# Performance work log

Measured on AMD Instinct MI355X. Metric: run time of the kernel, lower is better.

Reference implementation:

```python
import jax, jax.numpy as jnp
import numpy as np

ALPHA = 0.5  # ent message step size
BETA = 0.5   # rel message step size
N_ENT, N_REL, D, E = 100000, 500, 128, 1000000
EPS = 1e-12  # tf.math.l2_normalize epsilon


def _mul_complex(x, y):
    # interleaved complex multiply: even idx = real, odd idx = imag (RotatE)
    xr, xi = x[:, ::2], x[:, 1::2]
    yr, yi = y[:, ::2], y[:, 1::2]
    rr = xr * yr - xi * yi
    ri = xi * yr + xr * yi
    return jnp.stack([rr, ri], axis=2).reshape(x.shape[0], -1)


def _l2_normalize_pairs(r):
    # tf.math.l2_normalize over each (real, imag) pair
    r2 = r.reshape(-1, 2)
    denom = jnp.sqrt(jnp.maximum(jnp.sum(r2 * r2, axis=1, keepdims=True), EPS))
    return (r2 / denom).reshape(r.shape)


def setup_inputs() -> dict:
    key = jax.random.key(0)
    k = jax.random.split(key, 7)
    return {
        "ent_emb": jax.random.normal(k[0], (N_ENT, D), dtype=jnp.float32),
        "rel_emb": jax.random.normal(k[1], (N_REL, D), dtype=jnp.float32),
        "ent_invsum": jax.random.uniform(k[2], (N_ENT, 1), dtype=jnp.float32),
        "rel_invsum": jax.random.uniform(k[3], (N_REL, 1), dtype=jnp.float32),
        "head": jax.random.randint(k[4], (E,), 0, N_ENT, dtype=jnp.int32),
        "rel_idx": jax.random.randint(k[5], (E,), 0, N_REL, dtype=jnp.int32),
        "tail": jax.random.randint(k[6], (E,), 0, N_ENT, dtype=jnp.int32),
    }


def reference(ent_emb, rel_emb, ent_invsum, rel_invsum, head, rel_idx, tail):
    # RotatE mode: normalize each complex component of relation embeddings
    rel_n = _l2_normalize_pairs(rel_emb)

    def loss_fn(e, r):
        h = e[head]            # [E, D] gather
        t = e[tail]            # [E, D] gather
        rg = r[rel_idx]        # [E, D] gather
        return -jnp.sum((_mul_complex(h, rg) - t) ** 2)

    # tf.gradients(loss, [ent_emb, rel_emb]) -> scatter-add messages
    ent_msg, rel_msg = jax.grad(loss_fn, argnums=(0, 1))(ent_emb, rel_n)

    out_ent = jax.nn.relu(ent_emb + ALPHA * ent_invsum * ent_msg)
    out_rel = jax.nn.relu(rel_n + BETA * rel_invsum * rel_msg)
    return out_ent, out_rel
```

## Files before the change

kernel.cpp:

```cpp
#include <hip/hip_runtime.h>

#define N_ENT   100000
#define N_REL   500
#define DIM     128
#define NPAIR   64
#define CAP_E   36
#define NREP    8
#define CAP_RR  344
#define BIN_SH  5
#define NBIN    (N_ENT >> BIN_SH)
#define CAP_B   152
#define BS_THR  1024
#define MAXE    8
#define NCOPY   8
#define ALPHA   0.5f
#define BETA    0.5f
#define EPS_N   1e-12f
#define PMASK   0x1FFFFu
#define PAYMASK 0x03FFFFFFu
#define INVALID 0xFFFFFFFFu

__device__ __forceinline__ unsigned get_xcc() {
    unsigned x;
    asm("s_getreg_b32 %0, hwreg(HW_REG_XCC_ID)" : "=s"(x));
    return x & (NREP - 1u);
}

__device__ __forceinline__ unsigned pack_bf16(float2 v) {
    unsigned rx = __float_as_uint(v.x);
    unsigned ry = __float_as_uint(v.y);
    rx = (rx + 0x7FFFu + ((rx >> 16) & 1u)) >> 16;
    ry = (ry + 0x7FFFu + ((ry >> 16) & 1u)) & 0xFFFF0000u;
    return rx | ry;
}
__device__ __forceinline__ float2 unpack_bf16(unsigned u) {
    float2 v;
    v.x = __uint_as_float(u << 16);
    v.y = __uint_as_float(u & 0xFFFF0000u);
    return v;
}

__device__ __forceinline__ unsigned short pack_fp8(float2 v) {
    int p = __builtin_amdgcn_cvt_pk_fp8_f32(v.x, v.y, 0, false);
    return (unsigned short)(p & 0xFFFF);
}
__device__ __forceinline__ float2 unpack_fp8(unsigned short u) {
    float2 v;
    v.x = __builtin_amdgcn_cvt_f32_fp8((int)u, 0);
    v.y = __builtin_amdgcn_cvt_f32_fp8((int)u, 1);
    return v;
}

__global__ void zero_kernel(float* p, int n) {
    int i = blockIdx.x * blockDim.x + threadIdx.x;
    if (i < n) p[i] = 0.0f;
}

__global__ void cvt_ent_kernel(const float* __restrict__ ent, unsigned short* __restrict__ ent_f8, int npairs) {
    int i = blockIdx.x * blockDim.x + threadIdx.x;
    if (i >= npairs) return;
    ent_f8[i] = pack_fp8(reinterpret_cast<const float2*>(ent)[i]);
}

__global__ void rel_norm_kernel(const float* __restrict__ rel, float* __restrict__ rel_n,
                                unsigned* __restrict__ rel_bf, int npairs) {
    int i = blockIdx.x * blockDim.x + threadIdx.x;
    if (i >= npairs) return;
    float2 v = reinterpret_cast<const float2*>(rel)[i];
    float d = sqrtf(fmaxf(v.x * v.x + v.y * v.y, EPS_N));
    float2 o; o.x = v.x / d; o.y = v.y / d;
    reinterpret_cast<float2*>(rel_n)[i] = o;
    rel_bf[i] = pack_bf16(o);
}


__global__ __launch_bounds__(BS_THR) void bin_scatter(
                            const int* __restrict__ head,
                            const int* __restrict__ relidx,
                            const int* __restrict__ tail,
                            unsigned* __restrict__ bin_cnt,
                            unsigned* __restrict__ bins,
                            unsigned* __restrict__ deg_r,
                            uint2*    __restrict__ list_r,
                            int n_edge) {
    __shared__ unsigned lcnt[NBIN];
    __shared__ unsigned lbase[NBIN];
    __shared__ unsigned rcnt[N_REL];
    __shared__ unsigned rbase[N_REL];
    int tid = threadIdx.x;

    for (int i = tid; i < NBIN; i += BS_THR) lcnt[i] = 0;
    for (int i = tid; i < N_REL; i += BS_THR) rcnt[i] = 0;
    __syncthreads();

    int e0 = blockIdx.x * (MAXE * BS_THR);

    unsigned eh[MAXE], er[MAXE], et[MAXE];
#pragma unroll
    for (int i = 0; i < MAXE; ++i) {
        int e = e0 + tid + i * BS_THR;
        if (e < n_edge) {
            eh[i] = (unsigned)head[e];
            er[i] = (unsigned)relidx[e];
            et[i] = (unsigned)tail[e];
        } else {
            eh[i] = INVALID; er[i] = 0; et[i] = 0;
        }
    }

#pragma unroll
    for (int i = 0; i < MAXE; ++i) {
        if (eh[i] != INVALID) {
            atomicAdd(&lcnt[et[i] >> BIN_SH], 1u);
            atomicAdd(&lcnt[eh[i] >> BIN_SH], 1u);
            atomicAdd(&rcnt[er[i]], 1u);
        }
    }
    __syncthreads();

    unsigned rep = get_xcc();
    for (int b = tid; b < NBIN; b += BS_THR) {
        unsigned c = lcnt[b];
        if (c) lbase[b] = __hip_atomic_fetch_add(&bin_cnt[rep * NBIN + b], c,
                                                 __ATOMIC_RELAXED, __HIP_MEMORY_SCOPE_WORKGROUP);
    }
    for (int b = tid; b < N_REL; b += BS_THR) {
        unsigned c = rcnt[b];
        if (c) rbase[b] = __hip_atomic_fetch_add(&deg_r[rep * N_REL + b], c,
                                                 __ATOMIC_RELAXED, __HIP_MEMORY_SCOPE_WORKGROUP);
    }
    __syncthreads();

#pragma unroll
    for (int i = 0; i < MAXE; ++i) {
        if (eh[i] == INVALID) continue;
        unsigned h = eh[i], r = er[i], t = et[i];

        unsigned bt = t >> BIN_SH;
        unsigned s1 = lbase[bt] + (atomicSub(&lcnt[bt], 1u) - 1u);
        if (s1 < CAP_B) bins[((size_t)rep * NBIN + bt) * CAP_B + s1] = ((t & 31u) << 27) | (r << 17) | h;

        unsigned bh = h >> BIN_SH;
        unsigned s2 = lbase[bh] + (atomicSub(&lcnt[bh], 1u) - 1u);
        if (s2 < CAP_B) bins[((size_t)rep * NBIN + bh) * CAP_B + s2] = ((h & 31u) << 27) | (1u << 26) | (r << 17) | t;

        unsigned s3 = rbase[r] + (atomicSub(&rcnt[r], 1u) - 1u);
        if (s3 < CAP_RR) list_r[((size_t)rep * N_REL + r) * CAP_RR + s3] = make_uint2(h, t);
    }
}

__global__ void fused_ent(const float* __restrict__ ent,
                          const unsigned short* __restrict__ ent_f8,
                          const unsigned* __restrict__ rel_bf,
                          const unsigned* __restrict__ bin_cnt,
                          const unsigned* __restrict__ bins,
                          const float* __restrict__ ent_inv,
                          float* __restrict__ out_ent) {
    __shared__ unsigned cnt[32][2];
    __shared__ unsigned slots[32][2][CAP_E];
    int bin = blockIdx.x;
    int tid = threadIdx.x;

    if (tid < 64) cnt[tid >> 1][tid & 1] = 0;
    __syncthreads();

    for (int rep = 0; rep < NREP; ++rep) {
        int bn = (int)min(bin_cnt[(size_t)rep * NBIN + bin], (unsigned)CAP_B);
        for (int k = tid; k < bn; k += blockDim.x) {
            unsigned entry = bins[((size_t)rep * NBIN + bin) * CAP_B + k];
            unsigned el   = entry >> 27;
            unsigned role = (entry >> 26) & 1u;
            unsigned pay  = entry & PAYMASK;
            unsigned p = atomicAdd(&cnt[el][role], 1u);
            if (p < CAP_E) slots[el][role][p] = pay;
        }
    }
    __syncthreads();

    int wid  = tid >> 6;
    int lane = tid & 63;
    const float2* ent2 = reinterpret_cast<const float2*>(ent);

    for (int s = 0; s < 8; ++s) {
        int el = wid * 8 + s;
        int e  = (bin << BIN_SH) + el;
        int dt = (int)min(cnt[el][0], (unsigned)CAP_E);
        int dh = (int)min(cnt[el][1], (unsigned)CAP_E);

        float2 acc = make_float2(0.f, 0.f);
        for (int j = 0; j < dt; ++j) {
            unsigned ep = slots[el][0][j];
            float2 hv = unpack_fp8(ent_f8[(size_t)(ep & PMASK) * NPAIR + lane]);
            float2 rv = unpack_bf16(rel_bf[(size_t)(ep >> 17) * NPAIR + lane]);
            acc.x += hv.x * rv.x - hv.y * rv.y;
            acc.y += hv.y * rv.x + hv.x * rv.y;
        }
        for (int j = 0; j < dh; ++j) {
            unsigned ep = slots[el][1][j];
            float2 tv = unpack_fp8(ent_f8[(size_t)(ep & PMASK) * NPAIR + lane]);
            float2 rv = unpack_bf16(rel_bf[(size_t)(ep >> 17) * NPAIR + lane]);
            acc.x += tv.x * rv.x + tv.y * rv.y;
            acc.y += tv.y * rv.x - tv.x * rv.y;
        }

        float2 ev = ent2[(size_t)e * NPAIR + lane];
        float degf = (float)(dt + dh);
        float a = ALPHA * ent_inv[e];
        float2 o;
        o.x = fmaxf(ev.x + a * 2.f * (acc.x - degf * ev.x), 0.f);
        o.y = fmaxf(ev.y + a * 2.f * (acc.y - degf * ev.y), 0.f);
        reinterpret_cast<float2*>(out_ent)[(size_t)e * NPAIR + lane] = o;
    }
}

__global__ void rel_pass8(const unsigned short* __restrict__ ent_f8,
                          const unsigned* __restrict__ deg_r,
                          const uint2* __restrict__ list_r,
                          float* __restrict__ rel_part) {
    __shared__ float sh[4][NPAIR][3];
    int r   = blockIdx.x >> 3;
    int rep = blockIdx.x & 7;
    int wid = threadIdx.x >> 6;
    int lane = threadIdx.x & 63;
    int nr = (int)min(deg_r[(size_t)rep * N_REL + r], (unsigned)CAP_RR);

    const uint2* seg = list_r + ((size_t)rep * N_REL + r) * CAP_RR;

    float2 T0 = make_float2(0.f, 0.f), T1 = make_float2(0.f, 0.f);
    float S0 = 0.f, S1 = 0.f;
    for (int k = wid * 2; k < nr; k += 8) {
        uint2 e0 = seg[k];
        float2 hv0 = unpack_fp8(ent_f8[(size_t)e0.x * NPAIR + lane]);
        float2 tv0 = unpack_fp8(ent_f8[(size_t)e0.y * NPAIR + lane]);
        if (k + 1 < nr) {
            uint2 e1 = seg[k + 1];
            float2 hv1 = unpack_fp8(ent_f8[(size_t)e1.x * NPAIR + lane]);
            float2 tv1 = unpack_fp8(ent_f8[(size_t)e1.y * NPAIR + lane]);
            S1   += hv1.x * hv1.x + hv1.y * hv1.y;
            T1.x += tv1.x * hv1.x + tv1.y * hv1.y;
            T1.y += tv1.y * hv1.x - tv1.x * hv1.y;
        }
        S0   += hv0.x * hv0.x + hv0.y * hv0.y;
        T0.x += tv0.x * hv0.x + tv0.y * hv0.y;
        T0.y += tv0.y * hv0.x - tv0.x * hv0.y;
    }
    sh[wid][lane][0] = T0.x + T1.x;
    sh[wid][lane][1] = T0.y + T1.y;
    sh[wid][lane][2] = S0 + S1;
    __syncthreads();
    if (wid == 0) {
        float tx = 0.f, ty = 0.f, s = 0.f;
#pragma unroll
        for (int w = 0; w < 4; ++w) {
            tx += sh[w][lane][0];
            ty += sh[w][lane][1];
            s  += sh[w][lane][2];
        }
        size_t o = (((size_t)r * NREP + rep) * NPAIR + lane) * 3;
        rel_part[o + 0] = tx;
        rel_part[o + 1] = ty;
        rel_part[o + 2] = s;
    }
}

__global__ void rel_fin(const float* __restrict__ rel_n,
                        const float* __restrict__ rel_part,
                        const float* __restrict__ rel_inv,
                        float* __restrict__ out_rel) {
    int r = blockIdx.x;
    int lane = threadIdx.x;
    float tx = 0.f, ty = 0.f, s = 0.f;
#pragma unroll
    for (int rep = 0; rep < NREP; ++rep) {
        size_t o = (((size_t)r * NREP + rep) * NPAIR + lane) * 3;
        tx += rel_part[o + 0];
        ty += rel_part[o + 1];
        s  += rel_part[o + 2];
    }
    float2 rn = reinterpret_cast<const float2*>(rel_n)[(size_t)r * NPAIR + lane];
    float b = BETA * rel_inv[r];
    float2 o2;
    o2.x = fmaxf(rn.x + b * (-2.f) * (rn.x * s - tx), 0.f);
    o2.y = fmaxf(rn.y + b * (-2.f) * (rn.y * s - ty), 0.f);
    reinterpret_cast<float2*>(out_rel)[(size_t)r * NPAIR + lane] = o2;
}


__global__ void rel_norm_only(const float* __restrict__ rel, float* __restrict__ rel_n, int npairs) {
    int i = blockIdx.x * blockDim.x + threadIdx.x;
    if (i >= npairs) return;
    float2 v = reinterpret_cast<const float2*>(rel)[i];
    float d = sqrtf(fmaxf(v.x * v.x + v.y * v.y, EPS_N));
    float2 o; o.x = v.x / d; o.y = v.y / d;
    reinterpret_cast<float2*>(rel_n)[i] = o;
}

__global__ void edge_kernel(const float* __restrict__ ent,
                            const float* __restrict__ rel_n,
                            const int* __restrict__ head,
                            const int* __restrict__ relidx,
                            const int* __restrict__ tail,
                            float* __restrict__ ent_msg,
                            float* __restrict__ rel_msg,
                            int n_edge) {
    int gid  = blockIdx.x * blockDim.x + threadIdx.x;
    int eid  = gid >> 6;
    int lane = threadIdx.x & 63;
    if (eid >= n_edge) return;

    int h = head[eid];
    int t = tail[eid];
    int r = relidx[eid];

    float2 hv = reinterpret_cast<const float2*>(ent)[(size_t)h * 64 + lane];
    float2 tv = reinterpret_cast<const float2*>(ent)[(size_t)t * 64 + lane];
    float2 rv = reinterpret_cast<const float2*>(rel_n)[(size_t)r * 64 + lane];

    float mr = hv.x * rv.x - hv.y * rv.y;
    float mi = hv.y * rv.x + hv.x * rv.y;
    float dr = mr - tv.x;
    float di = mi - tv.y;

    atomicAdd(&ent_msg[(size_t)t * DIM + 2 * lane],     2.0f * dr);
    atomicAdd(&ent_msg[(size_t)t * DIM + 2 * lane + 1], 2.0f * di);
    atomicAdd(&ent_msg[(size_t)h * DIM + 2 * lane],     -2.0f * (dr * rv.x + di * rv.y));
    atomicAdd(&ent_msg[(size_t)h * DIM + 2 * lane + 1], -2.0f * (di * rv.x - dr * rv.y));

    float* rm = rel_msg + (size_t)(blockIdx.x & (NCOPY - 1)) * (N_REL * DIM);
    atomicAdd(&rm[(size_t)r * DIM + 2 * lane],     -2.0f * (dr * hv.x + di * hv.y));
    atomicAdd(&rm[(size_t)r * DIM + 2 * lane + 1], -2.0f * (di * hv.x - dr * hv.y));
}

__global__ void fin_ent_kernel(const float* __restrict__ ent,
                               const float* __restrict__ invsum,
                               float* __restrict__ out, int nvec4) {
    int i = blockIdx.x * blockDim.x + threadIdx.x;
    if (i >= nvec4) return;
    int row = i >> 5;
    float a = ALPHA * invsum[row];
    float4 m = reinterpret_cast<const float4*>(out)[i];
    float4 e = reinterpret_cast<const float4*>(ent)[i];
    float4 o;
    o.x = fmaxf(e.x + a * m.x, 0.0f);
    o.y = fmaxf(e.y + a * m.y, 0.0f);
    o.z = fmaxf(e.z + a * m.z, 0.0f);
    o.w = fmaxf(e.w + a * m.w, 0.0f);
    reinterpret_cast<float4*>(out)[i] = o;
}

__global__ void fin_rel_kernel(const float* __restrict__ rel_n,
                               const float* __restrict__ invsum,
                               const float* __restrict__ rel_msg,
                               float* __restrict__ out, int n) {
    int i = blockIdx.x * blockDim.x + threadIdx.x;
    if (i >= n) return;
    int row = i >> 7;
    float s = 0.0f;
#pragma unroll
    for (int c = 0; c < NCOPY; ++c) s += rel_msg[(size_t)c * (N_REL * DIM) + i];
    float o = rel_n[i] + BETA * invsum[row] * s;
    out[i] = fmaxf(o, 0.0f);
}

extern "C" void kernel_launch(void* const* d_in, const int* in_sizes, int n_in,
                              void* d_out, int out_size, void* d_ws, size_t ws_size,
                              hipStream_t stream) {
    const float* ent     = (const float*)d_in[0];
    const float* rel     = (const float*)d_in[1];
    const float* ent_inv = (const float*)d_in[2];
    const float* rel_inv = (const float*)d_in[3];
    const int*   head    = (const int*)d_in[4];
    const int*   relidx  = (const int*)d_in[5];
    const int*   tail    = (const int*)d_in[6];

    const int n_edge = in_sizes[4];

    float* out     = (float*)d_out;
    float* out_ent = out;
    float* out_rel = out + (size_t)N_ENT * DIM;

    const int B = 256;

    const size_t W_RELN  = 0;
    const size_t W_RELB  = W_RELN + (size_t)N_REL * NPAIR * 2;
    const size_t W_ENTF8 = W_RELB + (size_t)N_REL * NPAIR;
    const size_t W_BCNT  = W_ENTF8 + (size_t)N_ENT * NPAIR / 2;
    const size_t W_DEGR  = W_BCNT + (size_t)NREP * NBIN;
    const size_t W_RPART = W_DEGR + (size_t)NREP * N_REL;
    const size_t W_BINS  = W_RPART + (size_t)N_REL * NREP * NPAIR * 3;
    const size_t W_LISTR = W_BINS + (size_t)NREP * NBIN * CAP_B;
    const size_t W_END   = W_LISTR + (size_t)NREP * N_REL * CAP_RR * 2;
    const size_t need_fast = W_END * 4;

    float* ws = (float*)d_ws;

    if (ws_size >= need_fast) {
        float*          rel_n    = ws + W_RELN;
        unsigned*       rel_bf   = (unsigned*)(ws + W_RELB);
        unsigned short* ent_f8   = (unsigned short*)(ws + W_ENTF8);
        unsigned*       bin_cnt  = (unsigned*)(ws + W_BCNT);
        unsigned*       deg_r    = (unsigned*)(ws + W_DEGR);
        float*          rel_part = ws + W_RPART;
        unsigned*       bins     = (unsigned*)(ws + W_BINS);
        uint2*          list_r   = (uint2*)(ws + W_LISTR);

        hipMemsetAsync((void*)bin_cnt, 0,
                       (size_t)(NREP * NBIN + NREP * N_REL) * 4, stream);

        {
            int np = N_ENT * NPAIR;
            cvt_ent_kernel<<<(np + B - 1) / B, B, 0, stream>>>(ent, ent_f8, np);
        }
        {
            int npairs = N_REL * NPAIR;
            rel_norm_kernel<<<(npairs + B - 1) / B, B, 0, stream>>>(rel, rel_n, rel_bf, npairs);
        }
        {
            int nblk = (n_edge + MAXE * BS_THR - 1) / (MAXE * BS_THR);
            bin_scatter<<<nblk, BS_THR, 0, stream>>>(
                head, relidx, tail, bin_cnt, bins, deg_r, list_r, n_edge);
        }

        fused_ent<<<NBIN, B, 0, stream>>>(ent, ent_f8, rel_bf, bin_cnt, bins,
                                          ent_inv, out_ent);
        rel_pass8<<<N_REL * NREP, B, 0, stream>>>(ent_f8, deg_r, list_r, rel_part);
        rel_fin<<<N_REL, 64, 0, stream>>>(rel_n, rel_part, rel_inv, out_rel);
    } else {
        float* rel_n   = ws;
        float* rel_msg = ws + N_REL * DIM;

        {
            int n = N_ENT * DIM;
            zero_kernel<<<(n + B - 1) / B, B, 0, stream>>>(out_ent, n);
            int m = NCOPY * N_REL * DIM;
            zero_kernel<<<(m + B - 1) / B, B, 0, stream>>>(rel_msg, m);
        }
        {
            int npairs = N_REL * NPAIR;
            rel_norm_only<<<(npairs + B - 1) / B, B, 0, stream>>>(rel, rel_n, npairs);
        }
        {
            long long threads = (long long)n_edge * 64;
            int blocks = (int)((threads + B - 1) / B);
            edge_kernel<<<blocks, B, 0, stream>>>(ent, rel_n, head, relidx, tail,
                                                  out_ent, rel_msg, n_edge);
        }
        {
            int nvec4 = N_ENT * (DIM / 4);
            fin_ent_kernel<<<(nvec4 + B - 1) / B, B, 0, stream>>>(ent, ent_inv, out_ent, nvec4);
            int n = N_REL * DIM;
            fin_rel_kernel<<<(n + B - 1) / B, B, 0, stream>>>(rel_n, rel_inv, rel_msg, out_rel, n);
        }
    }
}
```

Baseline: 220.0 us.

## Widen per-lane loads in fused_ent and fp8 conversion; split edges across half-waves

fused_ent now has each half-wavefront handle alternate edges, with each lane loading two complex pairs (ushort2 fp8, uint2 bf16). The two halves are combined with a cross-half shuffle before a float4 write of the output row. The goal is fewer, wider memory transactions and two independent edge gathers in flight per wave. The fp8 conversion kernel now packs four floats per thread into one dword, and MAXE drops from 8 to 4, which doubles the number of bin_scatter blocks. The costs are an extra shuffle reduction, half the lanes sitting idle during the epilogue, and load imbalance when edge counts are odd.

```diff
diff --git a/kernel.cpp b/kernel.cpp
--- a/kernel.cpp
+++ b/kernel.cpp
@@ -11,7 +11,7 @@
 #define NBIN    (N_ENT >> BIN_SH)
 #define CAP_B   152
 #define BS_THR  1024
-#define MAXE    8
+#define MAXE    4
 #define NCOPY   8
 #define ALPHA   0.5f
 #define BETA    0.5f
@@ -40,10 +40,6 @@
     return v;
 }
 
-__device__ __forceinline__ unsigned short pack_fp8(float2 v) {
-    int p = __builtin_amdgcn_cvt_pk_fp8_f32(v.x, v.y, 0, false);
-    return (unsigned short)(p & 0xFFFF);
-}
 __device__ __forceinline__ float2 unpack_fp8(unsigned short u) {
     float2 v;
     v.x = __builtin_amdgcn_cvt_f32_fp8((int)u, 0);
@@ -56,10 +52,13 @@
     if (i < n) p[i] = 0.0f;
 }
 
-__global__ void cvt_ent_kernel(const float* __restrict__ ent, unsigned short* __restrict__ ent_f8, int npairs) {
-    int i = blockIdx.x * blockDim.x + threadIdx.x;
-    if (i >= npairs) return;
-    ent_f8[i] = pack_fp8(reinterpret_cast<const float2*>(ent)[i]);
+__global__ void cvt_ent_kernel(const float* __restrict__ ent, unsigned* __restrict__ ent_f8, int ndw) {
+    int i = blockIdx.x * blockDim.x + threadIdx.x;
+    if (i >= ndw) return;
+    float4 v = reinterpret_cast<const float4*>(ent)[i];
+    int p = __builtin_amdgcn_cvt_pk_fp8_f32(v.x, v.y, 0, false);
+    p = __builtin_amdgcn_cvt_pk_fp8_f32(v.z, v.w, p, true);
+    ent_f8[i] = (unsigned)p;
 }
 
 __global__ void rel_norm_kernel(const float* __restrict__ rel, float* __restrict__ rel_n,
@@ -179,7 +178,12 @@
 
     int wid  = tid >> 6;
     int lane = tid & 63;
-    const float2* ent2 = reinterpret_cast<const float2*>(ent);
+    int l31  = lane & 31;
+    int half = lane >> 5;
+
+    const float4*   ent4 = reinterpret_cast<const float4*>(ent);
+    const ushort2*  ef8  = reinterpret_cast<const ushort2*>(ent_f8);
+    const uint2*    rbf2 = reinterpret_cast<const uint2*>(rel_bf);
 
     for (int s = 0; s < 8; ++s) {
         int el = wid * 8 + s;
@@ -187,29 +191,47 @@
         int dt = (int)min(cnt[el][0], (unsigned)CAP_E);
         int dh = (int)min(cnt[el][1], (unsigned)CAP_E);
 
-        float2 acc = make_float2(0.f, 0.f);
-        for (int j = 0; j < dt; ++j) {
+        float4 acc = make_float4(0.f, 0.f, 0.f, 0.f);
+
+        for (int j = half; j < dt; j += 2) {
             unsigned ep = slots[el][0][j];
-            float2 hv = unpack_fp8(ent_f8[(size_t)(ep & PMASK) * NPAIR + lane]);
-            float2 rv = unpack_bf16(rel_bf[(size_t)(ep >> 17) * NPAIR + lane]);
-            acc.x += hv.x * rv.x - hv.y * rv.y;
-            acc.y += hv.y * rv.x + hv.x * rv.y;
-        }
-        for (int j = 0; j < dh; ++j) {
+            ushort2 hp = ef8[(size_t)(ep & PMASK) * 32 + l31];
+            uint2   rp = rbf2[(size_t)(ep >> 17) * 32 + l31];
+            float2 hv0 = unpack_fp8(hp.x), hv1 = unpack_fp8(hp.y);
+            float2 rv0 = unpack_bf16(rp.x), rv1 = unpack_bf16(rp.y);
+            acc.x += hv0.x * rv0.x - hv0.y * rv0.y;
+            acc.y += hv0.y * rv0.x + hv0.x * rv0.y;
+            acc.z += hv1.x * rv1.x - hv1.y * rv1.y;
+            acc.w += hv1.y * rv1.x + hv1.x * rv1.y;
+        }
+        for (int j = half; j < dh; j += 2) {
             unsigned ep = slots[el][1][j];
-            float2 tv = unpack_fp8(ent_f8[(size_t)(ep & PMASK) * NPAIR + lane]);
-            float2 rv = unpack_bf16(rel_bf[(size_t)(ep >> 17) * NPAIR + lane]);
-            acc.x += tv.x * rv.x + tv.y * rv.y;
-            acc.y += tv.y * rv.x - tv.x * rv.y;
-        }
-
-        float2 ev = ent2[(size_t)e * NPAIR + lane];
-        float degf = (float)(dt + dh);
-        float a = ALPHA * ent_inv[e];
-        float2 o;
-        o.x = fmaxf(ev.x + a * 2.f * (acc.x - degf * ev.x), 0.f);
-        o.y = fmaxf(ev.y + a * 2.f * (acc.y - degf * ev.y), 0.f);
-        reinterpret_cast<float2*>(out_ent)[(size_t)e * NPAIR + lane] = o;
+            ushort2 tp = ef8[(size_t)(ep & PMASK) * 32 + l31];
+            uint2   rp = rbf2[(size_t)(ep >> 17) * 32 + l31];
+            float2 tv0 = unpack_fp8(tp.x), tv1 = unpack_fp8(tp.y);
+            float2 rv0 = unpack_bf16(rp.x), rv1 = unpack_bf16(rp.y);
+            acc.x += tv0.x * rv0.x + tv0.y * rv0.y;
+            acc.y += tv0.y * rv0.x - tv0.x * rv0.y;
+            acc.z += tv1.x * rv1.x + tv1.y * rv1.y;
+            acc.w += tv1.y * rv1.x - tv1.x * rv1.y;
+        }
+
+        acc.x += __shfl_xor(acc.x, 32);
+        acc.y += __shfl_xor(acc.y, 32);
+        acc.z += __shfl_xor(acc.z, 32);
+        acc.w += __shfl_xor(acc.w, 32);
+
+        if (half == 0) {
+            float4 ev = ent4[(size_t)e * 32 + l31];
+            float degf = (float)(dt + dh);
+            float a = ALPHA * ent_inv[e];
+            float4 o;
+            o.x = fmaxf(ev.x + a * 2.f * (acc.x - degf * ev.x), 0.f);
+            o.y = fmaxf(ev.y + a * 2.f * (acc.y - degf * ev.y), 0.f);
+            o.z = fmaxf(ev.z + a * 2.f * (acc.z - degf * ev.z), 0.f);
+            o.w = fmaxf(ev.w + a * 2.f * (acc.w - degf * ev.w), 0.f);
+            reinterpret_cast<float4*>(out_ent)[(size_t)e * 32 + l31] = o;
+        }
     }
 }
 
@@ -408,8 +430,8 @@
                        (size_t)(NREP * NBIN + NREP * N_REL) * 4, stream);
 
         {
-            int np = N_ENT * NPAIR;
-            cvt_ent_kernel<<<(np + B - 1) / B, B, 0, stream>>>(ent, ent_f8, np);
+            int ndw = N_ENT * DIM / 4;
+            cvt_ent_kernel<<<(ndw + B - 1) / B, B, 0, stream>>>(ent, (unsigned*)ent_f8, ndw);
         }
         {
             int npairs = N_REL * NPAIR;
```

Result: no change. 220.6 us (+0.3%).
